# Kernel optimization log

Hardware: AMD Instinct MI355X
Metric: run time of the kernel (lower is better)

The kernel has to match this reference:

```python
import jax, jax.numpy as jnp
import numpy as np
import math

E = 256      # emb_size
H = 4        # num_heads
D = E // H   # head_dim
EXPLORE_SCALE = 0.5
EXPLOIT_SCALE = 0.5
TEMP_MIN = 0.5
TEMP_MAX = 2.0


def setup_inputs() -> dict:
    key = jax.random.key(0)
    ks = jax.random.split(key, 12)
    B, S = 4, 2048
    his_emb = jax.random.normal(ks[0], (B, S, E), dtype=jnp.float32)
    src_key_padding_mask = jax.random.randint(ks[1], (B, S), 0, 2) > 0
    explore = jax.random.uniform(ks[2], (B, S), dtype=jnp.float32)
    exploit = jax.random.uniform(ks[3], (B, S), dtype=jnp.float32)
    scale = 1.0 / math.sqrt(E)
    Wq = jax.random.normal(ks[4], (E, E), dtype=jnp.float32) * scale
    bq = jnp.zeros((E,), dtype=jnp.float32)
    Wk = jax.random.normal(ks[5], (E, E), dtype=jnp.float32) * scale
    bk = jnp.zeros((E,), dtype=jnp.float32)
    Wv = jax.random.normal(ks[6], (E, E), dtype=jnp.float32) * scale
    bv = jnp.zeros((E,), dtype=jnp.float32)
    Wo = jax.random.normal(ks[7], (E, E), dtype=jnp.float32) * scale
    bo = jnp.zeros((E,), dtype=jnp.float32)
    return {"his_emb": his_emb, "src_key_padding_mask": src_key_padding_mask,
            "explore": explore, "exploit": exploit,
            "Wq": Wq, "bq": bq, "Wk": Wk, "bk": bk,
            "Wv": Wv, "bv": bv, "Wo": Wo, "bo": bo}


def reference(his_emb, src_key_padding_mask, explore, exploit,
              Wq, bq, Wk, bk, Wv, bv, Wo, bo):
    B, S, _ = his_emb.shape
    # projections -> [B, H, S, D]
    q = (his_emb @ Wq + bq).reshape(B, S, H, D).transpose(0, 2, 1, 3)
    k = (his_emb @ Wk + bk).reshape(B, S, H, D).transpose(0, 2, 1, 3)
    v = (his_emb @ Wv + bv).reshape(B, S, H, D).transpose(0, 2, 1, 3)
    logits = jnp.einsum('bhqd,bhkd->bhqk', q, k) / math.sqrt(D)
    attn_mask = src_key_padding_mask[:, None, None, :]  # [B,1,1,S] over keys
    logits = jnp.where(attn_mask, -1e16, logits)
    # per-query dynamic temperature
    temp = 1.0 + EXPLORE_SCALE * explore - EXPLOIT_SCALE * exploit  # [B,S]
    temp = jnp.clip(temp, TEMP_MIN, TEMP_MAX)
    temp = jnp.where(src_key_padding_mask, 1.0, temp)
    logits = logits / temp[:, None, :, None]
    probs = jax.nn.softmax(logits, axis=-1)
    probs = jnp.where(attn_mask, 0.0, probs)
    probs = probs / jnp.maximum(probs.sum(axis=-1, keepdims=True), 1e-8)
    out = jnp.einsum('bhqk,bhkd->bhqd', probs, v)
    out = out.transpose(0, 2, 1, 3).reshape(B, S, E)
    out = out @ Wo + bo
    return jnp.where(src_key_padding_mask[:, :, None], 0.0, out)
```

## Files before the change

kernel.cpp:

```cpp
#include <hip/hip_runtime.h>
#include <hip/hip_bf16.h>
#include <math.h>

#define B_ 4
#define S_ 2048
#define E_ 256
#define H_ 4
#define D_ 64
#define NROW (B_*S_)
#define NCH 4
#define CHK (S_/NCH)
#define FM 12.0f

typedef __attribute__((ext_vector_type(8))) short short8;
typedef __attribute__((ext_vector_type(4))) float floatx4;

__device__ __forceinline__ short f2bf(float f){
    union{float f; unsigned u;} x; x.f = f;
    unsigned r = x.u + 0x7fffu + ((x.u>>16)&1u);
    return (short)(r>>16);
}
__device__ __forceinline__ float bf2f(short s){
    union{unsigned u; float f;} x; x.u = ((unsigned)(unsigned short)s)<<16; return x.f;
}
__device__ __forceinline__ unsigned pk_trunc(float lo, float hi){
    return __builtin_amdgcn_perm(__float_as_uint(hi), __float_as_uint(lo), 0x07060302u);
}

__global__ __launch_bounds__(256) void transpose_w(
    const float* __restrict__ W0, const float* __restrict__ W1,
    const float* __restrict__ W2, const float* __restrict__ W3,
    short* __restrict__ T0, short* __restrict__ T1,
    short* __restrict__ T2, short* __restrict__ T3)
{
    const float* W = blockIdx.y==0?W0: blockIdx.y==1?W1: blockIdx.y==2?W2:W3;
    short*       T = blockIdx.y==0?T0: blockIdx.y==1?T1: blockIdx.y==2?T2:T3;
    __shared__ float L[64][65];
    const int t = threadIdx.x;
    const int k0 = (blockIdx.x>>2)*64, n0 = (blockIdx.x&3)*64;
    {
        int r = t>>2, c0 = (t&3)*16;
        const float4* p = (const float4*)(W + (size_t)(k0+r)*E_ + n0 + c0);
        #pragma unroll
        for (int j=0;j<4;++j){
            float4 u = p[j];
            L[r][c0+4*j]=u.x; L[r][c0+4*j+1]=u.y; L[r][c0+4*j+2]=u.z; L[r][c0+4*j+3]=u.w;
        }
    }
    __syncthreads();
    {
        int n = t>>2, kk0 = (t&3)*16;
        short8 o0, o1;
        #pragma unroll
        for(int j=0;j<8;++j) o0[j] = f2bf(L[kk0+j][n]);
        #pragma unroll
        for(int j=0;j<8;++j) o1[j] = f2bf(L[kk0+8+j][n]);
        short* dst = T + (size_t)(n0+n)*E_ + k0 + kk0;
        *(short8*)dst = o0; *(short8*)(dst+8) = o1;
    }
}

__global__ __launch_bounds__(256) void qkv_gemm(
    const float* __restrict__ X,
    const short* __restrict__ Wtq, const float* __restrict__ bq,
    const short* __restrict__ Wtk, const float* __restrict__ bk,
    const short* __restrict__ Wtv, const float* __restrict__ bv,
    const int* __restrict__ mask,
    const float* __restrict__ explore, const float* __restrict__ exploit,
    short* __restrict__ Q, short* __restrict__ K, short* __restrict__ Vt)
{
    __shared__ __align__(16) short As[64][72];
    __shared__ __align__(16) short BsQ[64][72];
    __shared__ __align__(16) short BsK[64][72];
    __shared__ __align__(16) short BsV[64][72];

    const int t=threadIdx.x, w=t>>6, lane=t&63, ln=lane&15, quad=lane>>4;
    const int m0 = blockIdx.y*64, n0 = blockIdx.x*64;

    floatx4 aq[4] = {}, ak[4] = {}, av[4] = {};
    for (int kt=0; kt<E_; kt+=64){
        __syncthreads();
        {
            int r=t>>2, c0=(t&3)*16;
            const float4* pa = (const float4*)(X + (size_t)(m0+r)*E_ + kt + c0);
            short8 s0, s1;
            float4 u;
            u=pa[0]; s0[0]=f2bf(u.x); s0[1]=f2bf(u.y); s0[2]=f2bf(u.z); s0[3]=f2bf(u.w);
            u=pa[1]; s0[4]=f2bf(u.x); s0[5]=f2bf(u.y); s0[6]=f2bf(u.z); s0[7]=f2bf(u.w);
            u=pa[2]; s1[0]=f2bf(u.x); s1[1]=f2bf(u.y); s1[2]=f2bf(u.z); s1[3]=f2bf(u.w);
            u=pa[3]; s1[4]=f2bf(u.x); s1[5]=f2bf(u.y); s1[6]=f2bf(u.z); s1[7]=f2bf(u.w);
            *(short8*)&As[r][c0] = s0; *(short8*)&As[r][c0+8] = s1;
            size_t woff = (size_t)(n0+r)*E_ + kt + c0;
            const uint4* pq = (const uint4*)(Wtq + woff);
            *(uint4*)&BsQ[r][c0] = pq[0]; *(uint4*)&BsQ[r][c0+8] = pq[1];
            const uint4* pk = (const uint4*)(Wtk + woff);
            *(uint4*)&BsK[r][c0] = pk[0]; *(uint4*)&BsK[r][c0+8] = pk[1];
            const uint4* pv = (const uint4*)(Wtv + woff);
            *(uint4*)&BsV[r][c0] = pv[0]; *(uint4*)&BsV[r][c0+8] = pv[1];
        }
        __syncthreads();
        short8 a0 = *(const short8*)&As[w*16+ln][quad*8];
        short8 a1 = *(const short8*)&As[w*16+ln][32+quad*8];
        #pragma unroll
        for (int c=0;c<4;++c){
            short8 b0 = *(const short8*)&BsQ[c*16+ln][quad*8];
            short8 b1 = *(const short8*)&BsQ[c*16+ln][32+quad*8];
            aq[c] = __builtin_amdgcn_mfma_f32_16x16x32_bf16(a0,b0,aq[c],0,0,0);
            aq[c] = __builtin_amdgcn_mfma_f32_16x16x32_bf16(a1,b1,aq[c],0,0,0);
            b0 = *(const short8*)&BsK[c*16+ln][quad*8];
            b1 = *(const short8*)&BsK[c*16+ln][32+quad*8];
            ak[c] = __builtin_amdgcn_mfma_f32_16x16x32_bf16(a0,b0,ak[c],0,0,0);
            ak[c] = __builtin_amdgcn_mfma_f32_16x16x32_bf16(a1,b1,ak[c],0,0,0);
            b0 = *(const short8*)&BsV[c*16+ln][quad*8];
            b1 = *(const short8*)&BsV[c*16+ln][32+quad*8];
            av[c] = __builtin_amdgcn_mfma_f32_16x16x32_bf16(a0,b0,av[c],0,0,0);
            av[c] = __builtin_amdgcn_mfma_f32_16x16x32_bf16(a1,b1,av[c],0,0,0);
        }
    }
    {
        float tscr[4];
        #pragma unroll
        for(int reg=0;reg<4;++reg){
            int row = m0 + w*16 + quad*4 + reg;
            float ex = explore[row], xp = exploit[row];
            float tmp = fminf(fmaxf(1.0f + 0.5f*ex - 0.5f*xp, 0.5f), 2.0f);
            tscr[reg] = mask[row] ? 0.125f : 1.0f/(8.0f*tmp);
        }
        #pragma unroll
        for(int c=0;c<4;++c){
            int colg = n0 + c*16 + ln;
            float bia = bq[colg];
            #pragma unroll
            for(int reg=0;reg<4;++reg){
                int row = m0 + w*16 + quad*4 + reg;
                Q[(size_t)row*E_ + colg] = f2bf((aq[c][reg] + bia)*tscr[reg]);
            }
        }
    }
    #pragma unroll
    for(int c=0;c<4;++c){
        int colg = n0 + c*16 + ln;
        float bia = bk[colg];
        #pragma unroll
        for(int reg=0;reg<4;++reg){
            int row = m0 + w*16 + quad*4 + reg;
            K[(size_t)row*E_ + colg] = f2bf(ak[c][reg] + bia);
        }
    }
    #pragma unroll
    for(int c=0;c<4;++c){
        int colg = n0 + c*16 + ln;
        int hx = colg>>6, d = colg&63;
        float bia = bv[colg];
        #pragma unroll
        for(int reg=0;reg<4;++reg){
            int row = m0 + w*16 + quad*4 + reg;
            int bb = row>>11, s = row&(S_-1);
            Vt[((size_t)((bb*H_+hx)*D_+d))*S_ + s] = f2bf(av[c][reg] + bia);
        }
    }
}

__global__ __launch_bounds__(256) void attn_mfma(
    const short* __restrict__ Qb, const short* __restrict__ Kb, const short* __restrict__ Vtb,
    const int* __restrict__ mask,
    short* __restrict__ OP, float* __restrict__ Lb)
{
    const int bh = blockIdx.z;
    const int b = bh>>2, h = bh&3;
    const int q0 = blockIdx.x*64;
    const int ck = blockIdx.y, k0 = ck*CHK;
    const int t=threadIdx.x, w=t>>6, lane=t&63, ln=lane&15, quad=lane>>4;

    __shared__ __align__(16) short Ks[64][72];
    __shared__ __align__(16) short Vs[64][72];
    __shared__ __align__(16) short Ps[4][16][72];
    __shared__ float mv[64];

    const short* qr = Qb + (size_t)(b*S_ + q0 + w*16 + ln)*E_ + h*D_;
    short8 qb0 = *(const short8*)(qr + quad*8);
    short8 qb1 = *(const short8*)(qr + 32 + quad*8);

    const int sr = t>>2, sc0 = (t&3)*16;
    const short* kgl = Kb + (size_t)(b*S_ + sr)*E_ + h*D_ + sc0;
    const short* vgl = Vtb + ((size_t)(bh*D_ + sr))*S_ + sc0;

    floatx4 of[4] = {};
    float lacc = 0.0f;

    for (int kt=k0; kt<k0+CHK; kt+=64){
        __syncthreads();
        {
            const uint4* gk = (const uint4*)(kgl + (size_t)kt*E_);
            *(uint4*)&Ks[sr][sc0] = gk[0]; *(uint4*)&Ks[sr][sc0+8] = gk[1];
            const uint4* gv = (const uint4*)(vgl + kt);
            *(uint4*)&Vs[sr][sc0] = gv[0]; *(uint4*)&Vs[sr][sc0+8] = gv[1];
        }
        if (t<64) mv[t] = (mask[b*S_+kt+t] ? -1e30f : 0.0f) - FM;
        __syncthreads();

        #pragma unroll
        for (int c=0;c<4;++c){
            short8 ka0 = *(const short8*)&Ks[c*16+ln][quad*8];
            short8 ka1 = *(const short8*)&Ks[c*16+ln][32+quad*8];
            float4 mvv = *(const float4*)&mv[c*16+quad*4];
            floatx4 s = {};
            s = __builtin_amdgcn_mfma_f32_16x16x32_bf16(ka0, qb0, s, 0,0,0);
            s = __builtin_amdgcn_mfma_f32_16x16x32_bf16(ka1, qb1, s, 0,0,0);
            float p0 = __expf(s[0] + mvv.x);
            float p1 = __expf(s[1] + mvv.y);
            float p2 = __expf(s[2] + mvv.z);
            float p3 = __expf(s[3] + mvv.w);
            lacc += (p0+p1)+(p2+p3);
            uint2 pw; pw.x = pk_trunc(p0,p1); pw.y = pk_trunc(p2,p3);
            *(uint2*)&Ps[w][ln][c*16+quad*4] = pw;
        }

        #pragma unroll
        for (int half=0; half<2; ++half){
            short8 pa = *(const short8*)&Ps[w][ln][half*32 + quad*8];
            #pragma unroll
            for (int dc=0; dc<4; ++dc){
                short8 vb = *(const short8*)&Vs[dc*16+ln][half*32 + quad*8];
                of[dc] = __builtin_amdgcn_mfma_f32_16x16x32_bf16(pa, vb, of[dc], 0,0,0);
            }
        }
    }

    float l = lacc;
    l += __shfl_xor(l, 16);
    l += __shfl_xor(l, 32);
    #pragma unroll
    for (int dc=0; dc<4; ++dc){
        #pragma unroll
        for (int reg=0; reg<4; ++reg){
            int q = q0 + w*16 + quad*4 + reg;
            OP[((size_t)(ck*16 + bh)*S_ + q)*D_ + dc*16 + ln] = f2bf(of[dc][reg]);
        }
    }
    if (quad==0)
        Lb[(size_t)(ck*16 + bh)*S_ + q0 + w*16 + ln] = l;
}

__global__ __launch_bounds__(256) void out_gemm(
    const short* __restrict__ OP, const float* __restrict__ Lb,
    const short* __restrict__ Wto, const float* __restrict__ bo,
    const int* __restrict__ mask, float* __restrict__ out)
{
    __shared__ __align__(16) short As[64][72];
    __shared__ __align__(16) short Bs[64][72];
    const int t=threadIdx.x, w=t>>6, lane=t&63, ln=lane&15, quad=lane>>4;
    const int m0 = blockIdx.y*64, n0 = blockIdx.x*64;
    const int r = t>>2, c0 = (t&3)*16;
    const int row = m0 + r, bq = row>>11, s = row&(S_-1);

    floatx4 acc[4] = {};
    for (int kt=0; kt<E_; kt+=64){
        __syncthreads();
        {
            int h = kt>>6, bh_ = bq*H_ + h;
            float osum[16]; float lsum = 0.f;
            #pragma unroll
            for (int j=0;j<16;++j) osum[j] = 0.f;
            #pragma unroll
            for (int cc=0; cc<NCH; ++cc){
                const uint4* p = (const uint4*)(OP + ((size_t)(cc*16 + bh_)*S_ + s)*D_ + c0);
                uint4 u0 = p[0], u1 = p[1];
                const short* sp0 = (const short*)&u0;
                const short* sp1 = (const short*)&u1;
                #pragma unroll
                for (int j=0;j<8;++j){ osum[j] += bf2f(sp0[j]); osum[8+j] += bf2f(sp1[j]); }
                lsum += Lb[(size_t)(cc*16 + bh_)*S_ + s];
            }
            float linv = 1.0f / fmaxf(lsum, 1e-8f);
            short8 s0, s1;
            #pragma unroll
            for (int j=0;j<8;++j){ s0[j] = f2bf(osum[j]*linv); s1[j] = f2bf(osum[8+j]*linv); }
            *(short8*)&As[r][c0] = s0; *(short8*)&As[r][c0+8] = s1;
            const uint4* pb = (const uint4*)(Wto + (size_t)(n0+r)*E_ + kt + c0);
            *(uint4*)&Bs[r][c0] = pb[0]; *(uint4*)&Bs[r][c0+8] = pb[1];
        }
        __syncthreads();
        short8 a0 = *(const short8*)&As[w*16+ln][quad*8];
        short8 a1 = *(const short8*)&As[w*16+ln][32+quad*8];
        #pragma unroll
        for (int c=0;c<4;++c){
            short8 b0 = *(const short8*)&Bs[c*16+ln][quad*8];
            short8 b1 = *(const short8*)&Bs[c*16+ln][32+quad*8];
            acc[c] = __builtin_amdgcn_mfma_f32_16x16x32_bf16(a0,b0,acc[c],0,0,0);
            acc[c] = __builtin_amdgcn_mfma_f32_16x16x32_bf16(a1,b1,acc[c],0,0,0);
        }
    }
    #pragma unroll
    for(int c=0;c<4;++c){
        int colg = n0 + c*16 + ln;
        float bia = bo[colg];
        #pragma unroll
        for(int reg=0;reg<4;++reg){
            int rowg = m0 + w*16 + quad*4 + reg;
            out[(size_t)rowg*E_ + colg] = mask[rowg] ? 0.0f : (acc[c][reg] + bia);
        }
    }
}

extern "C" void kernel_launch(void* const* d_in, const int* in_sizes, int n_in,
                              void* d_out, int out_size, void* d_ws, size_t ws_size,
                              hipStream_t stream) {
    const float* his     = (const float*)d_in[0];
    const int*   mask    = (const int*)d_in[1];
    const float* explore = (const float*)d_in[2];
    const float* exploit = (const float*)d_in[3];
    const float* Wq = (const float*)d_in[4];
    const float* bq = (const float*)d_in[5];
    const float* Wk = (const float*)d_in[6];
    const float* bk = (const float*)d_in[7];
    const float* Wv = (const float*)d_in[8];
    const float* bv = (const float*)d_in[9];
    const float* Wo = (const float*)d_in[10];
    const float* bo = (const float*)d_in[11];

    char* ws = (char*)d_ws;
    const size_t NE2 = (size_t)NROW * E_ * 2;
    short* Wtq  = (short*)(ws);                    ws += E_*E_*2;
    short* Wtk  = (short*)(ws);                    ws += E_*E_*2;
    short* Wtv  = (short*)(ws);                    ws += E_*E_*2;
    short* Wto  = (short*)(ws);                    ws += E_*E_*2;
    short* Qb   = (short*)(ws);                    ws += NE2;
    short* Kb   = (short*)(ws);                    ws += NE2;
    short* Vtb  = (short*)(ws);                    ws += NE2;
    short* OP   = (short*)(ws);                    ws += (size_t)NCH*B_*H_*S_*D_*2;
    float* Lb   = (float*)(ws);                    ws += (size_t)NCH*B_*H_*S_*4;

    transpose_w<<<dim3(16,4), 256, 0, stream>>>(Wq, Wk, Wv, Wo, Wtq, Wtk, Wtv, Wto);

    qkv_gemm<<<dim3(E_/64, NROW/64), 256, 0, stream>>>(
        his, Wtq, bq, Wtk, bk, Wtv, bv, mask, explore, exploit, Qb, Kb, Vtb);

    attn_mfma<<<dim3(S_/64, NCH, B_*H_), 256, 0, stream>>>(
        Qb, Kb, Vtb, mask, OP, Lb);

    out_gemm<<<dim3(E_/64, NROW/64), 256, 0, stream>>>(OP, Lb, Wto, bo, mask, (float*)d_out);
}
```

Baseline: 151.1 us.

## Split QKV gemm across grid z, double attention key chunks, add combine kernel

The QKV projection now launches one block per (tile, projection) along grid z instead of computing all three in one block. This triples the block count and cuts shared memory and accumulator registers per block, at the cost of converting X to bf16 three times. Attention key splitting goes from 4 to 8 chunks for more parallelism, and the mask bias for the whole chunk is loaded into shared memory once. The split-K reduction moves out of the output GEMM into a separate combine kernel that writes a bf16 context buffer reusing the Q buffer. The output GEMM then no longer recomputes the reduction for each of its 4 column tiles, but the change adds a launch and more partial-output traffic.

Measured after the change: 149.8 us. Within noise of the previous version (-0.9%).

```diff
diff --git a/kernel.cpp b/kernel.cpp
--- a/kernel.cpp
+++ b/kernel.cpp
@@ -8,7 +8,7 @@
 #define H_ 4
 #define D_ 64
 #define NROW (B_*S_)
-#define NCH 4
+#define NCH 8
 #define CHK (S_/NCH)
 #define FM 12.0f
 
@@ -69,15 +69,17 @@
     const float* __restrict__ explore, const float* __restrict__ exploit,
     short* __restrict__ Q, short* __restrict__ K, short* __restrict__ Vt)
 {
+    const int z = blockIdx.z;
+    const short* Wt   = z==0?Wtq: z==1?Wtk:Wtv;
+    const float* bias = z==0?bq:  z==1?bk:bv;
+
     __shared__ __align__(16) short As[64][72];
-    __shared__ __align__(16) short BsQ[64][72];
-    __shared__ __align__(16) short BsK[64][72];
-    __shared__ __align__(16) short BsV[64][72];
+    __shared__ __align__(16) short Bs[64][72];
 
     const int t=threadIdx.x, w=t>>6, lane=t&63, ln=lane&15, quad=lane>>4;
     const int m0 = blockIdx.y*64, n0 = blockIdx.x*64;
 
-    floatx4 aq[4] = {}, ak[4] = {}, av[4] = {};
+    floatx4 acc[4] = {};
     for (int kt=0; kt<E_; kt+=64){
         __syncthreads();
         {
@@ -90,34 +92,21 @@
             u=pa[2]; s1[0]=f2bf(u.x); s1[1]=f2bf(u.y); s1[2]=f2bf(u.z); s1[3]=f2bf(u.w);
             u=pa[3]; s1[4]=f2bf(u.x); s1[5]=f2bf(u.y); s1[6]=f2bf(u.z); s1[7]=f2bf(u.w);
             *(short8*)&As[r][c0] = s0; *(short8*)&As[r][c0+8] = s1;
-            size_t woff = (size_t)(n0+r)*E_ + kt + c0;
-            const uint4* pq = (const uint4*)(Wtq + woff);
-            *(uint4*)&BsQ[r][c0] = pq[0]; *(uint4*)&BsQ[r][c0+8] = pq[1];
-            const uint4* pk = (const uint4*)(Wtk + woff);
-            *(uint4*)&BsK[r][c0] = pk[0]; *(uint4*)&BsK[r][c0+8] = pk[1];
-            const uint4* pv = (const uint4*)(Wtv + woff);
-            *(uint4*)&BsV[r][c0] = pv[0]; *(uint4*)&BsV[r][c0+8] = pv[1];
+            const uint4* pb = (const uint4*)(Wt + (size_t)(n0+r)*E_ + kt + c0);
+            *(uint4*)&Bs[r][c0] = pb[0]; *(uint4*)&Bs[r][c0+8] = pb[1];
         }
         __syncthreads();
         short8 a0 = *(const short8*)&As[w*16+ln][quad*8];
         short8 a1 = *(const short8*)&As[w*16+ln][32+quad*8];
         #pragma unroll
         for (int c=0;c<4;++c){
-            short8 b0 = *(const short8*)&BsQ[c*16+ln][quad*8];
-            short8 b1 = *(const short8*)&BsQ[c*16+ln][32+quad*8];
-            aq[c] = __builtin_amdgcn_mfma_f32_16x16x32_bf16(a0,b0,aq[c],0,0,0);
-            aq[c] = __builtin_amdgcn_mfma_f32_16x16x32_bf16(a1,b1,aq[c],0,0,0);
-            b0 = *(const short8*)&BsK[c*16+ln][quad*8];
-            b1 = *(const short8*)&BsK[c*16+ln][32+quad*8];
-            ak[c] = __builtin_amdgcn_mfma_f32_16x16x32_bf16(a0,b0,ak[c],0,0,0);
-            ak[c] = __builtin_amdgcn_mfma_f32_16x16x32_bf16(a1,b1,ak[c],0,0,0);
-            b0 = *(const short8*)&BsV[c*16+ln][quad*8];
-            b1 = *(const short8*)&BsV[c*16+ln][32+quad*8];
-            av[c] = __builtin_amdgcn_mfma_f32_16x16x32_bf16(a0,b0,av[c],0,0,0);
-            av[c] = __builtin_amdgcn_mfma_f32_16x16x32_bf16(a1,b1,av[c],0,0,0);
-        }
-    }
-    {
+            short8 b0 = *(const short8*)&Bs[c*16+ln][quad*8];
+            short8 b1 = *(const short8*)&Bs[c*16+ln][32+quad*8];
+            acc[c] = __builtin_amdgcn_mfma_f32_16x16x32_bf16(a0,b0,acc[c],0,0,0);
+            acc[c] = __builtin_amdgcn_mfma_f32_16x16x32_bf16(a1,b1,acc[c],0,0,0);
+        }
+    }
+    if (z==0){
         float tscr[4];
         #pragma unroll
         for(int reg=0;reg<4;++reg){
@@ -129,34 +118,36 @@
         #pragma unroll
         for(int c=0;c<4;++c){
             int colg = n0 + c*16 + ln;
-            float bia = bq[colg];
+            float bia = bias[colg];
             #pragma unroll
             for(int reg=0;reg<4;++reg){
                 int row = m0 + w*16 + quad*4 + reg;
-                Q[(size_t)row*E_ + colg] = f2bf((aq[c][reg] + bia)*tscr[reg]);
+                Q[(size_t)row*E_ + colg] = f2bf((acc[c][reg] + bia)*tscr[reg]);
             }
         }
-    }
-    #pragma unroll
-    for(int c=0;c<4;++c){
-        int colg = n0 + c*16 + ln;
-        float bia = bk[colg];
-        #pragma unroll
-        for(int reg=0;reg<4;++reg){
-            int row = m0 + w*16 + quad*4 + reg;
-            K[(size_t)row*E_ + colg] = f2bf(ak[c][reg] + bia);
-        }
-    }
-    #pragma unroll
-    for(int c=0;c<4;++c){
-        int colg = n0 + c*16 + ln;
-        int hx = colg>>6, d = colg&63;
-        float bia = bv[colg];
-        #pragma unroll
-        for(int reg=0;reg<4;++reg){
-            int row = m0 + w*16 + quad*4 + reg;
-            int bb = row>>11, s = row&(S_-1);
-            Vt[((size_t)((bb*H_+hx)*D_+d))*S_ + s] = f2bf(av[c][reg] + bia);
+    } else if (z==1){
+        #pragma unroll
+        for(int c=0;c<4;++c){
+            int colg = n0 + c*16 + ln;
+            float bia = bias[colg];
+            #pragma unroll
+            for(int reg=0;reg<4;++reg){
+                int row = m0 + w*16 + quad*4 + reg;
+                K[(size_t)row*E_ + colg] = f2bf(acc[c][reg] + bia);
+            }
+        }
+    } else {
+        #pragma unroll
+        for(int c=0;c<4;++c){
+            int colg = n0 + c*16 + ln;
+            int hx = colg>>6, d = colg&63;
+            float bia = bias[colg];
+            #pragma unroll
+            for(int reg=0;reg<4;++reg){
+                int row = m0 + w*16 + quad*4 + reg;
+                int bb = row>>11, s = row&(S_-1);
+                Vt[((size_t)((bb*H_+hx)*D_+d))*S_ + s] = f2bf(acc[c][reg] + bia);
+            }
         }
     }
 }
@@ -175,7 +166,9 @@
     __shared__ __align__(16) short Ks[64][72];
     __shared__ __align__(16) short Vs[64][72];
     __shared__ __align__(16) short Ps[4][16][72];
-    __shared__ float mv[64];
+    __shared__ float mvAll[CHK];
+
+    if (t < CHK) mvAll[t] = (mask[b*S_ + k0 + t] ? -1e30f : 0.0f) - FM;
 
     const short* qr = Qb + (size_t)(b*S_ + q0 + w*16 + ln)*E_ + h*D_;
     short8 qb0 = *(const short8*)(qr + quad*8);
@@ -196,14 +189,13 @@
             const uint4* gv = (const uint4*)(vgl + kt);
             *(uint4*)&Vs[sr][sc0] = gv[0]; *(uint4*)&Vs[sr][sc0+8] = gv[1];
         }
-        if (t<64) mv[t] = (mask[b*S_+kt+t] ? -1e30f : 0.0f) - FM;
         __syncthreads();
 
         #pragma unroll
         for (int c=0;c<4;++c){
             short8 ka0 = *(const short8*)&Ks[c*16+ln][quad*8];
             short8 ka1 = *(const short8*)&Ks[c*16+ln][32+quad*8];
-            float4 mvv = *(const float4*)&mv[c*16+quad*4];
+            float4 mvv = *(const float4*)&mvAll[(kt-k0) + c*16+quad*4];
             floatx4 s = {};
             s = __builtin_amdgcn_mfma_f32_16x16x32_bf16(ka0, qb0, s, 0,0,0);
             s = __builtin_amdgcn_mfma_f32_16x16x32_bf16(ka1, qb1, s, 0,0,0);
@@ -242,41 +234,49 @@
         Lb[(size_t)(ck*16 + bh)*S_ + q0 + w*16 + ln] = l;
 }
 
+__global__ __launch_bounds__(256) void combine(
+    const short* __restrict__ OP, const float* __restrict__ Lb, short* __restrict__ CTXb)
+{
+    int gid = blockIdx.x*256 + threadIdx.x;
+    int e8 = gid & 31;
+    int row = gid >> 5;
+    int e = e8*8;
+    int hh = e >> 6, d0 = e & 63;
+    int bb = row >> 11, s = row & (S_-1);
+    int bh = bb*H_ + hh;
+
+    float osum[8] = {};
+    float lsum = 0.f;
+    #pragma unroll
+    for (int c=0;c<NCH;++c){
+        uint4 u = *(const uint4*)(OP + ((size_t)(c*16 + bh)*S_ + s)*D_ + d0);
+        const short* sp = (const short*)&u;
+        #pragma unroll
+        for (int j=0;j<8;++j) osum[j] += bf2f(sp[j]);
+        lsum += Lb[(size_t)(c*16 + bh)*S_ + s];
+    }
+    float linv = 1.0f / fmaxf(lsum, 1e-8f);
+    short8 o;
+    #pragma unroll
+    for (int j=0;j<8;++j) o[j] = f2bf(osum[j]*linv);
+    *(short8*)(CTXb + (size_t)row*E_ + e) = o;
+}
+
 __global__ __launch_bounds__(256) void out_gemm(
-    const short* __restrict__ OP, const float* __restrict__ Lb,
-    const short* __restrict__ Wto, const float* __restrict__ bo,
+    const short* __restrict__ Ab, const short* __restrict__ Wto, const float* __restrict__ bo,
     const int* __restrict__ mask, float* __restrict__ out)
 {
     __shared__ __align__(16) short As[64][72];
     __shared__ __align__(16) short Bs[64][72];
     const int t=threadIdx.x, w=t>>6, lane=t&63, ln=lane&15, quad=lane>>4;
     const int m0 = blockIdx.y*64, n0 = blockIdx.x*64;
-    const int r = t>>2, c0 = (t&3)*16;
-    const int row = m0 + r, bq = row>>11, s = row&(S_-1);
-
     floatx4 acc[4] = {};
     for (int kt=0; kt<E_; kt+=64){
         __syncthreads();
         {
-            int h = kt>>6, bh_ = bq*H_ + h;
-            float osum[16]; float lsum = 0.f;
-            #pragma unroll
-            for (int j=0;j<16;++j) osum[j] = 0.f;
-            #pragma unroll
-            for (int cc=0; cc<NCH; ++cc){
-                const uint4* p = (const uint4*)(OP + ((size_t)(cc*16 + bh_)*S_ + s)*D_ + c0);
-                uint4 u0 = p[0], u1 = p[1];
-                const short* sp0 = (const short*)&u0;
-                const short* sp1 = (const short*)&u1;
-                #pragma unroll
-                for (int j=0;j<8;++j){ osum[j] += bf2f(sp0[j]); osum[8+j] += bf2f(sp1[j]); }
-                lsum += Lb[(size_t)(cc*16 + bh_)*S_ + s];
-            }
-            float linv = 1.0f / fmaxf(lsum, 1e-8f);
-            short8 s0, s1;
-            #pragma unroll
-            for (int j=0;j<8;++j){ s0[j] = f2bf(osum[j]*linv); s1[j] = f2bf(osum[8+j]*linv); }
-            *(short8*)&As[r][c0] = s0; *(short8*)&As[r][c0+8] = s1;
+            int r=t>>2, c0=(t&3)*16;
+            const uint4* pa = (const uint4*)(Ab + (size_t)(m0+r)*E_ + kt + c0);
+            *(uint4*)&As[r][c0] = pa[0]; *(uint4*)&As[r][c0+8] = pa[1];
             const uint4* pb = (const uint4*)(Wto + (size_t)(n0+r)*E_ + kt + c0);
             *(uint4*)&Bs[r][c0] = pb[0]; *(uint4*)&Bs[r][c0+8] = pb[1];
         }
@@ -297,8 +297,8 @@
         float bia = bo[colg];
         #pragma unroll
         for(int reg=0;reg<4;++reg){
-            int rowg = m0 + w*16 + quad*4 + reg;
-            out[(size_t)rowg*E_ + colg] = mask[rowg] ? 0.0f : (acc[c][reg] + bia);
+            int row = m0 + w*16 + quad*4 + reg;
+            out[(size_t)row*E_ + colg] = mask[row] ? 0.0f : (acc[c][reg] + bia);
         }
     }
 }
@@ -330,14 +330,17 @@
     short* Vtb  = (short*)(ws);                    ws += NE2;
     short* OP   = (short*)(ws);                    ws += (size_t)NCH*B_*H_*S_*D_*2;
     float* Lb   = (float*)(ws);                    ws += (size_t)NCH*B_*H_*S_*4;
+    short* CTXb = Qb;
 
     transpose_w<<<dim3(16,4), 256, 0, stream>>>(Wq, Wk, Wv, Wo, Wtq, Wtk, Wtv, Wto);
 
-    qkv_gemm<<<dim3(E_/64, NROW/64), 256, 0, stream>>>(
+    qkv_gemm<<<dim3(E_/64, NROW/64, 3), 256, 0, stream>>>(
         his, Wtq, bq, Wtk, bk, Wtv, bv, mask, explore, exploit, Qb, Kb, Vtb);
 
     attn_mfma<<<dim3(S_/64, NCH, B_*H_), 256, 0, stream>>>(
         Qb, Kb, Vtb, mask, OP, Lb);
 
-    out_gemm<<<dim3(E_/64, NROW/64), 256, 0, stream>>>(OP, Lb, Wto, bo, mask, (float*)d_out);
-}
+    combine<<<1024, 256, 0, stream>>>(OP, Lb, CTXb);
+
+    out_gemm<<<dim3(E_/64, NROW/64), 256, 0, stream>>>(CTXb, Wto, bo, mask, (float*)d_out);
+}
```
